# Performance work log

Measured on AMD Instinct MI355X. Metric: run time of the kernel, lower is better.

Reference implementation:

```python
import math
import jax, jax.numpy as jnp
import numpy as np

B, T, E, H = 4, 2048, 1024, 16
S = E // H
SCALE = 1.0 / math.sqrt(S)
LN_EPS = 1e-5


def setup_inputs() -> dict:
    key = jax.random.key(0)
    ks = jax.random.split(key, 5)
    w_std = 1.0 / math.sqrt(E)
    return {
        "x": jax.random.normal(ks[0], (B, T, E), jnp.float32),
        "Wq": jax.random.normal(ks[1], (E, E), jnp.float32) * w_std,
        "Wk": jax.random.normal(ks[2], (E, E), jnp.float32) * w_std,
        "Wv": jax.random.normal(ks[3], (E, E), jnp.float32) * w_std,
        "Wu": jax.random.normal(ks[4], (E, E), jnp.float32) * w_std,
        "bu": jnp.zeros((E,), jnp.float32),
        "q_gamma": jnp.ones((S,), jnp.float32),
        "q_beta": jnp.zeros((S,), jnp.float32),
        "k_gamma": jnp.ones((S,), jnp.float32),
        "k_beta": jnp.zeros((S,), jnp.float32),
    }


def _layernorm(x, gamma, beta):
    # normalize over last (head) dim, eps matches torch LayerNorm default
    mu = jnp.mean(x, axis=-1, keepdims=True)
    var = jnp.mean(jnp.square(x - mu), axis=-1, keepdims=True)
    return (x - mu) * jax.lax.rsqrt(var + LN_EPS) * gamma + beta


def reference(x, Wq, Wk, Wv, Wu, bu, q_gamma, q_beta, k_gamma, k_beta):
    b, t, e = x.shape
    h, s = H, S
    # torch Linear: y = x @ W^T ; split into heads [b, t, h, s]
    q = (x @ Wq.T).reshape(b, t, h, s)
    k = (x @ Wk.T).reshape(b, t, h, s)
    v = (x @ Wv.T).reshape(b, t, h, s)
    # kqnorm: LayerNorm over head dim s
    q = _layernorm(q, q_gamma, q_beta)
    k = _layernorm(k, k_gamma, k_beta)
    # scaled dot-product scores [b, h, t, t]
    dots = jnp.einsum("bthd,bThd->bhtT", q, k) * SCALE
    causal = jnp.tril(jnp.ones((t, t), dtype=bool))
    dots = jnp.where(causal, dots, jnp.finfo(dots.dtype).min)
    attn = jax.nn.softmax(dots, axis=-1)
    out = jnp.einsum("bhtT,bThd->bthd", attn, v).reshape(b, t, e)
    return out @ Wu.T + bu
```

## Files before the change

### kernel.cpp

```cpp
#include <hip/hip_runtime.h>
#include <hip/hip_bf16.h>
#include <stdint.h>
#include <stddef.h>


using bf16 = __hip_bfloat16;
typedef __attribute__((ext_vector_type(8))) short s16x8;
typedef __attribute__((ext_vector_type(4))) short s16x4;
typedef __attribute__((ext_vector_type(4))) float f32x4;

#define MFMA16(a, b, c) __builtin_amdgcn_mfma_f32_16x16x32_bf16((a), (b), (c), 0, 0, 0)

static __device__ __forceinline__ s16x8 ld8(const bf16* p) {
    return *reinterpret_cast<const s16x8*>(p);
}
static __device__ __forceinline__ s16x8 ld8s(const short* p) {
    return *reinterpret_cast<const s16x8*>(p);
}
static __device__ __forceinline__ s16x8 cvt8(const float* p) {
    f32x4 u = *reinterpret_cast<const f32x4*>(p);
    f32x4 v = *reinterpret_cast<const f32x4*>(p + 4);
    s16x8 r;
#pragma unroll
    for (int e = 0; e < 4; e++) {
        r[e]     = __builtin_bit_cast(short, __float2bfloat16(u[e]));
        r[e + 4] = __builtin_bit_cast(short, __float2bfloat16(v[e]));
    }
    return r;
}
static __device__ __forceinline__ unsigned int cvtpk(float lo, float hi) {
    unsigned int r;
    asm("v_cvt_pk_bf16_f32 %0, %1, %2" : "=v"(r) : "v"(lo), "v"(hi));
    return r;
}

static __device__ __forceinline__ void async16(short* lds, const bf16* g) {
    __builtin_amdgcn_global_load_lds(
        (const __attribute__((address_space(1))) unsigned int*)g,
        (__attribute__((address_space(3))) unsigned int*)lds, 16, 0, 0);
}

#define EE 1024

__global__ __launch_bounds__(256) void cvt_all(
    const float* __restrict__ w0, const float* __restrict__ w1,
    const float* __restrict__ w2, const float* __restrict__ w3,
    const float* __restrict__ x,
    bf16* __restrict__ o0, bf16* __restrict__ o1,
    bf16* __restrict__ o2, bf16* __restrict__ o3, bf16* __restrict__ xb)
{
    const int z = blockIdx.z;
    const float* s;
    bf16* d;
    if (z < 4) {
        s = (z == 0) ? w0 : (z == 1) ? w1 : (z == 2) ? w2 : w3;
        d = (z == 0) ? o0 : (z == 1) ? o1 : (z == 2) ? o2 : o3;
    } else {
        s = x  + (size_t)(z - 4) * 1048576;
        d = xb + (size_t)(z - 4) * 1048576;
    }
    size_t i = ((size_t)blockIdx.x * 256 + threadIdx.x) * 8;
    *reinterpret_cast<s16x8*>(d + i) = cvt8(s + i);
}

template <int AF32>
__global__ __launch_bounds__(256) void gemm_qkv_t(
    const float* __restrict__ xf, const bf16* __restrict__ xb,
    const bf16* __restrict__ Wq, const bf16* __restrict__ Wk, const bf16* __restrict__ Wv,
    bf16* __restrict__ Qb, bf16* __restrict__ Kb, bf16* __restrict__ Vb,
    const float* __restrict__ qg, const float* __restrict__ qbt,
    const float* __restrict__ kg, const float* __restrict__ kbt)
{
    const int z = blockIdx.z;
    const bf16* Bt = (z == 0) ? Wq : (z == 1) ? Wk : Wv;
    bf16* out      = (z == 0) ? Qb : (z == 1) ? Kb : Vb;
    const float* gamma = (z == 0) ? qg : kg;
    const float* beta  = (z == 0) ? qbt : kbt;
    const bool  ln     = (z < 2);
    const float oscale = (z == 0) ? 0.125f : 1.0f;

    constexpr int LASZ = AF32 ? 128 * 40 : 2 * 4096;
    __shared__ __align__(16) short lA[LASZ];
    __shared__ __align__(16) short lB[2 * 4096];

    const int tid  = threadIdx.x;
    const int lane = tid & 63;
    const int w    = tid >> 6;
    const int wr = w >> 1, wc = w & 1;
    const int lr = lane & 15, quad = lane >> 4;

    const int mi = blockIdx.x * 8 + (blockIdx.y & 7);
    const int ni = blockIdx.y >> 3;
    const int m0 = mi * 128;
    const int n0 = ni * 128;

    const int strow = w * 32 + (lane >> 2);
    const int stcol = (lane & 3) * 8;
    const bf16* bgl = Bt + (size_t)(n0 + strow) * EE + stcol;

    f32x4 acc[4][4];
#pragma unroll
    for (int i = 0; i < 4; i++)
#pragma unroll
        for (int j = 0; j < 4; j++) acc[i][j] = (f32x4){0.f, 0.f, 0.f, 0.f};

    if constexpr (AF32) {
        constexpr int SA = 40;
        const int sr  = tid >> 1;
        const int sc0 = (tid & 1) << 4;
        const float* ap = xf + (size_t)(m0 + sr) * EE + sc0;
        short* lap = lA + sr * SA + sc0;
        short* bl = lB + (w * 2) * 512;
        const short* lArd = lA + (wr * 64 + lr) * SA + quad * 8;
        const short* lBrd = lB + (wc * 64 + lr) * 32 + quad * 8;
        const bf16* bg = bgl;

        for (int kt = 0; kt < EE / 32; ++kt) {
            s16x8 a0 = cvt8(ap), a1 = cvt8(ap + 8);
            __syncthreads();
            *reinterpret_cast<s16x8*>(lap)     = a0;
            *reinterpret_cast<s16x8*>(lap + 8) = a1;
            async16(bl, bg);
            async16(bl + 512, bg + 16 * EE);
            ap += 32;
            bg += 32;
            __syncthreads();

            s16x8 af[4], bfr[4];
#pragma unroll
            for (int i = 0; i < 4; i++) af[i]  = ld8s(lArd + i * 16 * SA);
#pragma unroll
            for (int j = 0; j < 4; j++) bfr[j] = ld8s(lBrd + j * 16 * 32);
#pragma unroll
            for (int i = 0; i < 4; i++)
#pragma unroll
                for (int j = 0; j < 4; j++) acc[i][j] = MFMA16(af[i], bfr[j], acc[i][j]);
        }
    } else {
        const bf16* agl = xb + (size_t)(m0 + strow) * EE + stcol;
        short* const al0 = lA + w * 1024;
        short* const bl0 = lB + w * 1024;

#define QSTAGE(c, kt)                                                     \
    {                                                                     \
        short* al = al0 + (c) * 4096;                                     \
        short* bl = bl0 + (c) * 4096;                                     \
        const bf16* ag = agl + (kt) * 32;                                 \
        const bf16* bg = bgl + (kt) * 32;                                 \
        async16(al, ag); async16(al + 512, ag + 16 * EE);                 \
        async16(bl, bg); async16(bl + 512, bg + 16 * EE);                 \
    }

        QSTAGE(0, 0)
#pragma unroll 1
        for (int kt = 0; kt < EE / 32; ++kt) {
            const int c = kt & 1;
            if (kt < EE / 32 - 1) {
                QSTAGE(c ^ 1, kt + 1)
                asm volatile("s_waitcnt vmcnt(4)" ::: "memory");
            } else {
                asm volatile("s_waitcnt vmcnt(0)" ::: "memory");
            }
            __builtin_amdgcn_s_barrier();

            const short* lArd = lA + c * 4096 + (wr * 64 + lr) * 32 + quad * 8;
            const short* lBrd = lB + c * 4096 + (wc * 64 + lr) * 32 + quad * 8;
            s16x8 af[4], bfr[4];
#pragma unroll
            for (int i = 0; i < 4; i++) af[i]  = ld8s(lArd + i * 512);
#pragma unroll
            for (int j = 0; j < 4; j++) bfr[j] = ld8s(lBrd + j * 512);
            __builtin_amdgcn_sched_barrier(0);
            asm volatile("s_waitcnt lgkmcnt(0)" ::: "memory");
            __builtin_amdgcn_sched_barrier(0);
#pragma unroll
            for (int i = 0; i < 4; i++)
#pragma unroll
                for (int j = 0; j < 4; j++) acc[i][j] = MFMA16(af[i], bfr[j], acc[i][j]);
            __builtin_amdgcn_s_barrier();
        }
#undef QSTAGE
    }

    if (ln) {
        float g[4], bt[4];
#pragma unroll
        for (int j = 0; j < 4; j++) {
            g[j]  = gamma[j * 16 + lr];
            bt[j] = beta[j * 16 + lr];
        }
#pragma unroll
        for (int i = 0; i < 4; i++) {
#pragma unroll
            for (int r = 0; r < 4; r++) {
                float s1 = 0.f, s2 = 0.f;
#pragma unroll
                for (int j = 0; j < 4; j++) {
                    float v = acc[i][j][r];
                    s1 += v;
                    s2 += v * v;
                }
#pragma unroll
                for (int off = 1; off < 16; off <<= 1) {
                    s1 += __shfl_xor(s1, off);
                    s2 += __shfl_xor(s2, off);
                }
                float mu  = s1 * (1.f / 64.f);
                float var = s2 * (1.f / 64.f) - mu * mu;
                float rs  = rsqrtf(var + 1e-5f);
                int row = m0 + wr * 64 + i * 16 + quad * 4 + r;
#pragma unroll
                for (int j = 0; j < 4; j++) {
                    float v = ((acc[i][j][r] - mu) * rs * g[j] + bt[j]) * oscale;
                    out[(size_t)row * EE + n0 + wc * 64 + j * 16 + lr] = __float2bfloat16(v);
                }
            }
        }
    } else {
#pragma unroll
        for (int i = 0; i < 4; i++)
#pragma unroll
            for (int r = 0; r < 4; r++) {
                int row = m0 + wr * 64 + i * 16 + quad * 4 + r;
#pragma unroll
                for (int j = 0; j < 4; j++)
                    out[(size_t)row * EE + n0 + wc * 64 + j * 16 + lr] =
                        __float2bfloat16(acc[i][j][r]);
            }
    }
}

__global__ __launch_bounds__(512, 4) void flash(
    const bf16* __restrict__ Qb, const bf16* __restrict__ Kb,
    const bf16* __restrict__ Vb, bf16* __restrict__ Ob)
{
    const int flat = blockIdx.y * 8 + blockIdx.x;
    const int vid  = (flat & 7) * 64 + (flat >> 3);
    const int pr = vid & 7;
    const int bh = vid >> 3;
    const int b = bh >> 4, h = bh & 15;
    const int tid = threadIdx.x, lane = tid & 63, w = tid >> 6;
    const int lr = lane & 15, quad = lane >> 4;
    const size_t base = (size_t)b * 2048 * 1024 + h * 64;
    const float C  = 1.44269504088896340736f;
    const float M0 = 12.0f;

    __shared__ __align__(16) short VT[64 * 72];
    __shared__ __align__(16) short PT[128 * 72];
    __shared__ __align__(16) short KS[2][64 * 64];

    short* const prow = PT + (w * 16 + lr) * 72;
    const bf16* const kst = Kb + base + (size_t)(w * 8 + (lane >> 3)) * 1024 +
                            (((lane & 7) ^ (lane >> 3)) << 3);
    short* const kdst = &KS[0][0] + w * 512;
    const int kaddr0 = lr * 64 + ((quad ^ (lr & 7)) << 3);

#pragma unroll 1
    for (int ph = 0; ph < 2; ++ph) {
        const int qt = ph ? (15 - pr) : pr;
        const int tw = qt * 128 + w * 16;

        s16x8 qf[2];
#pragma unroll
        for (int ks = 0; ks < 2; ks++)
            qf[ks] = ld8(Qb + base + (size_t)(tw + lr) * 1024 + ks * 32 + quad * 8);

        f32x4 o[4];
#pragma unroll
        for (int j = 0; j < 4; j++) o[j] = (f32x4){0.f, 0.f, 0.f, 0.f};
        float lsum = 0.f;

        const int nkt = 2 * qt + 2;

        __syncthreads();
        s16x8 va0 = ld8(Vb + base + (size_t)lane * 1024 + w * 8);
        s16x8 vb0;
        async16(kdst, kst);

#define FTILE(KT, V0C, KCUR, V0N, KNXT)                                          \
    {                                                                            \
        const int kb = (KT) * 64;                                                \
        const bool active = (kb <= tw + 15);                                     \
        asm volatile("s_waitcnt vmcnt(0)" ::: "memory");      \
        __builtin_amdgcn_s_barrier();       \
        _Pragma("unroll")                                                        \
        for (int e = 0; e < 8; e++)                                              \
            VT[(w * 8 + e) * 72 + lane] = V0C[e];                                \
        const int kb2 = kb + 64;                                                 \
        if (kb2 < nkt * 64) {       \
            async16(kdst + (KNXT) * 4096, kst + (size_t)kb2 * 1024);             \
            V0N = ld8(Vb + base + (size_t)(kb2 + lane) * 1024 + w * 8);          \
        }                                                                        \
        if (active) {                                                            \
            const short* kc = &KS[KCUR][0];                                      \
            f32x4 sc[4];                                                         \
            _Pragma("unroll")                                                    \
            for (int jk = 0; jk < 4; jk++) sc[jk] = (f32x4){0.f, 0.f, 0.f, 0.f}; \
            __builtin_amdgcn_s_setprio(1);                                       \
            _Pragma("unroll")                                                    \
            for (int ks = 0; ks < 2; ks++)                                       \
                _Pragma("unroll")                                                \
                for (int jk = 0; jk < 4; jk++) {                                 \
                    s16x8 kf = ld8s(kc + jk * 1024 + (kaddr0 ^ (ks * 32)));      \
                    sc[jk] = MFMA16(kf, qf[ks], sc[jk]);                         \
                }                                                                \
            __builtin_amdgcn_s_setprio(0);                                       \
            if (kb + 63 > tw) {                  \
                const int qq = tw + lr;                                          \
                _Pragma("unroll")                                                \
                for (int jk = 0; jk < 4; jk++) {                                 \
                    const int k0 = kb + jk * 16 + quad * 4;                      \
                    float p0 = exp2f(fmaf(sc[jk][0], C, -M0));                   \
                    float p1 = exp2f(fmaf(sc[jk][1], C, -M0));                   \
                    float p2 = exp2f(fmaf(sc[jk][2], C, -M0));                   \
                    float p3 = exp2f(fmaf(sc[jk][3], C, -M0));                   \
                    if (k0 + 0 > qq) p0 = 0.f;                                   \
                    if (k0 + 1 > qq) p1 = 0.f;                                   \
                    if (k0 + 2 > qq) p2 = 0.f;                                   \
                    if (k0 + 3 > qq) p3 = 0.f;                                   \
                    lsum += (p0 + p1) + (p2 + p3);                               \
                    uint2 pk = {cvtpk(p0, p1), cvtpk(p2, p3)};                   \
                    *reinterpret_cast<uint2*>(prow + jk * 16 + quad * 4) = pk;   \
                }                                                                \
            } else {                                 \
                _Pragma("unroll")                                                \
                for (int jk = 0; jk < 4; jk++) {                                 \
                    float p0 = exp2f(fmaf(sc[jk][0], C, -M0));                   \
                    float p1 = exp2f(fmaf(sc[jk][1], C, -M0));                   \
                    float p2 = exp2f(fmaf(sc[jk][2], C, -M0));                   \
                    float p3 = exp2f(fmaf(sc[jk][3], C, -M0));                   \
                    lsum += (p0 + p1) + (p2 + p3);                               \
                    uint2 pk = {cvtpk(p0, p1), cvtpk(p2, p3)};                   \
                    *reinterpret_cast<uint2*>(prow + jk * 16 + quad * 4) = pk;   \
                }                                                                \
            }                                                                    \
        }                                                                        \
        asm volatile("s_waitcnt lgkmcnt(0)" ::: "memory");    \
        __builtin_amdgcn_s_barrier();                  \
        if (active) {                                                            \
            _Pragma("unroll")                                                    \
            for (int ks = 0; ks < 2; ks++) {                                     \
                s16x8 pf = ld8s(prow + ks * 32 + quad * 8);                      \
                s16x8 vf[4];                                                     \
                _Pragma("unroll")                                                \
                for (int j = 0; j < 4; j++)                                      \
                    vf[j] = ld8s(VT + (j * 16 + lr) * 72 + ks * 32 + quad * 8);  \
                __builtin_amdgcn_s_setprio(1);                                   \
                _Pragma("unroll")                                                \
                for (int j = 0; j < 4; j++)                                      \
                    o[j] = MFMA16(pf, vf[j], o[j]);                              \
                __builtin_amdgcn_s_setprio(0);                                   \
            }                                                                    \
        }                                                                        \
    }

#pragma unroll 1
        for (int kt = 0; kt < nkt; kt += 2) {
            FTILE(kt,     va0, 0, vb0, 1)
            FTILE(kt + 1, vb0, 1, va0, 0)
        }
#undef FTILE

        float l = lsum;
        l += __shfl_xor(l, 16);
        l += __shfl_xor(l, 32);
#pragma unroll
        for (int r = 0; r < 4; r++) {
            float inv = 1.f / __shfl(l, quad * 4 + r);
            int t = tw + quad * 4 + r;
#pragma unroll
            for (int j = 0; j < 4; j++)
                Ob[base + (size_t)t * 1024 + j * 16 + lr] =
                    __float2bfloat16(o[j][r] * inv);
        }
    }
}

__global__ __launch_bounds__(256) void gemm_bias(
    const bf16* __restrict__ A, const bf16* __restrict__ Bt,
    const float* __restrict__ bias, float* __restrict__ out)
{
    __shared__ __align__(16) short lA[2 * 4096];
    __shared__ __align__(16) short lB[2 * 4096];

    const int tid  = threadIdx.x;
    const int lane = tid & 63;
    const int w    = tid >> 6;
    const int wr = w >> 1, wc = w & 1;
    const int lr = lane & 15, quad = lane >> 4;

    const int mi = blockIdx.x * 8 + (blockIdx.y & 7);
    const int ni = blockIdx.y >> 3;
    const int m0 = mi * 128;
    const int n0 = ni * 128;

    const int strow = w * 32 + (lane >> 2);
    const int stcol = (lane & 3) * 8;
    const bf16* agl = A  + (size_t)(m0 + strow) * EE + stcol;
    const bf16* bgl = Bt + (size_t)(n0 + strow) * EE + stcol;
    short* const al0 = lA + w * 1024;
    short* const bl0 = lB + w * 1024;

    f32x4 acc[4][4];
#pragma unroll
    for (int i = 0; i < 4; i++)
#pragma unroll
        for (int j = 0; j < 4; j++) acc[i][j] = (f32x4){0.f, 0.f, 0.f, 0.f};

#define BSTAGE(c, kt)                                                     \
    {                                                                     \
        short* al = al0 + (c) * 4096;                                     \
        short* bl = bl0 + (c) * 4096;                                     \
        const bf16* ag = agl + (kt) * 32;                                 \
        const bf16* bg = bgl + (kt) * 32;                                 \
        async16(al, ag); async16(al + 512, ag + 16 * EE);                 \
        async16(bl, bg); async16(bl + 512, bg + 16 * EE);                 \
    }

    BSTAGE(0, 0)
#pragma unroll 1
    for (int kt = 0; kt < EE / 32; ++kt) {
        const int c = kt & 1;
        if (kt < EE / 32 - 1) {
            BSTAGE(c ^ 1, kt + 1)
            asm volatile("s_waitcnt vmcnt(4)" ::: "memory");
        } else {
            asm volatile("s_waitcnt vmcnt(0)" ::: "memory");
        }
        __builtin_amdgcn_s_barrier();

        const short* lArd = lA + c * 4096 + (wr * 64 + lr) * 32 + quad * 8;
        const short* lBrd = lB + c * 4096 + (wc * 64 + lr) * 32 + quad * 8;
        s16x8 af[4], bfr[4];
#pragma unroll
        for (int i = 0; i < 4; i++) af[i]  = ld8s(lArd + i * 512);
#pragma unroll
        for (int j = 0; j < 4; j++) bfr[j] = ld8s(lBrd + j * 512);
        __builtin_amdgcn_sched_barrier(0);
        asm volatile("s_waitcnt lgkmcnt(0)" ::: "memory");
        __builtin_amdgcn_sched_barrier(0);
#pragma unroll
        for (int i = 0; i < 4; i++)
#pragma unroll
            for (int j = 0; j < 4; j++) acc[i][j] = MFMA16(af[i], bfr[j], acc[i][j]);
        __builtin_amdgcn_s_barrier();
    }
#undef BSTAGE

    float bz[4];
#pragma unroll
    for (int j = 0; j < 4; j++)
        bz[j] = bias[n0 + wc * 64 + j * 16 + lr];
#pragma unroll
    for (int i = 0; i < 4; i++)
#pragma unroll
        for (int r = 0; r < 4; r++) {
            int row = m0 + wr * 64 + i * 16 + quad * 4 + r;
#pragma unroll
            for (int j = 0; j < 4; j++)
                out[(size_t)row * EE + n0 + wc * 64 + j * 16 + lr] =
                    acc[i][j][r] + bz[j];
        }
}

extern "C" void kernel_launch(void* const* d_in, const int* in_sizes, int n_in,
                              void* d_out, int out_size, void* d_ws, size_t ws_size,
                              hipStream_t stream)
{
    (void)in_sizes; (void)n_in; (void)out_size;
    const float* x   = (const float*)d_in[0];
    const float* Wq  = (const float*)d_in[1];
    const float* Wk  = (const float*)d_in[2];
    const float* Wv  = (const float*)d_in[3];
    const float* Wu  = (const float*)d_in[4];
    const float* bu  = (const float*)d_in[5];
    const float* qg  = (const float*)d_in[6];
    const float* qbt = (const float*)d_in[7];
    const float* kg  = (const float*)d_in[8];
    const float* kbt = (const float*)d_in[9];
    float* out = (float*)d_out;

    bf16* Qb  = (bf16*)d_ws;
    bf16* Kb  = Qb  + (size_t)8192 * 1024;
    bf16* Vb  = Kb  + (size_t)8192 * 1024;
    bf16* Wqb = Vb  + (size_t)8192 * 1024;
    bf16* Wkb = Wqb + (size_t)1024 * 1024;
    bf16* Wvb = Wkb + (size_t)1024 * 1024;
    bf16* Wub = Wvb + (size_t)1024 * 1024;
    bf16* xb  = Wub + (size_t)1024 * 1024;

    const size_t need = ((size_t)3 * 8192 * 1024 + 4 * 1024 * 1024 + 8192 * 1024) * 2;
    const bool fast = ws_size >= need;

    cvt_all<<<dim3(512, 1, fast ? 12 : 4), 256, 0, stream>>>(
        Wq, Wk, Wv, Wu, x, Wqb, Wkb, Wvb, Wub, xb);
    if (fast)
        gemm_qkv_t<0><<<dim3(8, 64, 3), 256, 0, stream>>>(
            x, xb, Wqb, Wkb, Wvb, Qb, Kb, Vb, qg, qbt, kg, kbt);
    else
        gemm_qkv_t<1><<<dim3(8, 64, 3), 256, 0, stream>>>(
            x, nullptr, Wqb, Wkb, Wvb, Qb, Kb, Vb, qg, qbt, kg, kbt);
    flash<<<dim3(8, 64), 512, 0, stream>>>(Qb, Kb, Vb, Qb);
    gemm_bias<<<dim3(8, 64), 256, 0, stream>>>(Qb, Wub, bu, out);
}
```

Baseline: 278.1 us.

## Split flash attention into 64-row query blocks with longest-first scheduling

The flash kernel moves from 512-thread blocks that each handle two paired 128-row query tiles to 256-thread blocks that each handle a single 64-row query tile. The grid grows from 512 to 2048 blocks, and query blocks are issued in descending order so the longest causal workloads start first. Each warp now loads twice as much K/V per tile, and the per-warp causal skip check is dropped. The aim is better load balance and occupancy from finer-grained work, at the cost of reloading K/V more often per query row, since each block has fewer query rows to reuse it.

```diff
diff --git a/kernel.cpp b/kernel.cpp
--- a/kernel.cpp
+++ b/kernel.cpp
@@ -230,14 +230,14 @@
     }
 }
 
-__global__ __launch_bounds__(512, 4) void flash(
+__global__ __launch_bounds__(256, 4) void flash(
     const bf16* __restrict__ Qb, const bf16* __restrict__ Kb,
     const bf16* __restrict__ Vb, bf16* __restrict__ Ob)
 {
-    const int flat = blockIdx.y * 8 + blockIdx.x;
-    const int vid  = (flat & 7) * 64 + (flat >> 3);
-    const int pr = vid & 7;
-    const int bh = vid >> 3;
+    const int flat = blockIdx.y * 32 + blockIdx.x;
+    const int vid  = (flat & 7) * 256 + (flat >> 3);
+    const int qb = 31 - (vid & 31);
+    const int bh = vid >> 5;
     const int b = bh >> 4, h = bh & 15;
     const int tid = threadIdx.x, lane = tid & 63, w = tid >> 6;
     const int lr = lane & 15, quad = lane >> 4;
@@ -246,52 +246,53 @@
     const float M0 = 12.0f;
 
     __shared__ __align__(16) short VT[64 * 72];
-    __shared__ __align__(16) short PT[128 * 72];
+    __shared__ __align__(16) short PT[64 * 72];
     __shared__ __align__(16) short KS[2][64 * 64];
 
     short* const prow = PT + (w * 16 + lr) * 72;
-    const bf16* const kst = Kb + base + (size_t)(w * 8 + (lane >> 3)) * 1024 +
+    const bf16* const kst = Kb + base + (size_t)(w * 16 + (lane >> 3)) * 1024 +
                             (((lane & 7) ^ (lane >> 3)) << 3);
-    short* const kdst = &KS[0][0] + w * 512;
+    short* const kdst = &KS[0][0] + w * 1024;
     const int kaddr0 = lr * 64 + ((quad ^ (lr & 7)) << 3);
 
-#pragma unroll 1
-    for (int ph = 0; ph < 2; ++ph) {
-        const int qt = ph ? (15 - pr) : pr;
-        const int tw = qt * 128 + w * 16;
-
-        s16x8 qf[2];
-#pragma unroll
-        for (int ks = 0; ks < 2; ks++)
-            qf[ks] = ld8(Qb + base + (size_t)(tw + lr) * 1024 + ks * 32 + quad * 8);
-
-        f32x4 o[4];
-#pragma unroll
-        for (int j = 0; j < 4; j++) o[j] = (f32x4){0.f, 0.f, 0.f, 0.f};
-        float lsum = 0.f;
-
-        const int nkt = 2 * qt + 2;
-
-        __syncthreads();
-        s16x8 va0 = ld8(Vb + base + (size_t)lane * 1024 + w * 8);
-        s16x8 vb0;
-        async16(kdst, kst);
-
-#define FTILE(KT, V0C, KCUR, V0N, KNXT)                                          \
+    const int tw = qb * 64 + w * 16;
+    const int nkt = qb + 1;
+
+    s16x8 qf[2];
+#pragma unroll
+    for (int ks = 0; ks < 2; ks++)
+        qf[ks] = ld8(Qb + base + (size_t)(tw + lr) * 1024 + ks * 32 + quad * 8);
+
+    f32x4 o[4];
+#pragma unroll
+    for (int j = 0; j < 4; j++) o[j] = (f32x4){0.f, 0.f, 0.f, 0.f};
+    float lsum = 0.f;
+
+    s16x8 va0 = ld8(Vb + base + (size_t)lane * 1024 + w * 8);
+    s16x8 va1 = ld8(Vb + base + (size_t)lane * 1024 + w * 8 + 32);
+    s16x8 vb0, vb1;
+    async16(kdst, kst);
+    async16(kdst + 512, kst + (size_t)8 * 1024);
+
+#define FTILE(KT, V0C, V1C, KCUR, V0N, V1N, KNXT)                                \
     {                                                                            \
         const int kb = (KT) * 64;                                                \
-        const bool active = (kb <= tw + 15);                                     \
         asm volatile("s_waitcnt vmcnt(0)" ::: "memory");      \
         __builtin_amdgcn_s_barrier();       \
         _Pragma("unroll")                                                        \
-        for (int e = 0; e < 8; e++)                                              \
-            VT[(w * 8 + e) * 72 + lane] = V0C[e];                                \
+        for (int e = 0; e < 8; e++) {                                            \
+            VT[(w * 8 + e) * 72 + lane]      = V0C[e];                           \
+            VT[(w * 8 + 32 + e) * 72 + lane] = V1C[e];                           \
+        }                                                                        \
         const int kb2 = kb + 64;                                                 \
         if (kb2 < nkt * 64) {       \
             async16(kdst + (KNXT) * 4096, kst + (size_t)kb2 * 1024);             \
+            async16(kdst + (KNXT) * 4096 + 512,                                  \
+                    kst + (size_t)(kb2 + 8) * 1024);                             \
             V0N = ld8(Vb + base + (size_t)(kb2 + lane) * 1024 + w * 8);          \
+            V1N = ld8(Vb + base + (size_t)(kb2 + lane) * 1024 + w * 8 + 32);     \
         }                                                                        \
-        if (active) {                                                            \
+        {                                                                        \
             const short* kc = &KS[KCUR][0];                                      \
             f32x4 sc[4];                                                         \
             _Pragma("unroll")                                                    \
@@ -337,7 +338,7 @@
         }                                                                        \
         asm volatile("s_waitcnt lgkmcnt(0)" ::: "memory");    \
         __builtin_amdgcn_s_barrier();                  \
-        if (active) {                                                            \
+        {                                                                        \
             _Pragma("unroll")                                                    \
             for (int ks = 0; ks < 2; ks++) {                                     \
                 s16x8 pf = ld8s(prow + ks * 32 + quad * 8);                      \
@@ -354,25 +355,28 @@
         }                                                                        \
     }
 
+    int kt = 0;
 #pragma unroll 1
-        for (int kt = 0; kt < nkt; kt += 2) {
-            FTILE(kt,     va0, 0, vb0, 1)
-            FTILE(kt + 1, vb0, 1, va0, 0)
-        }
+    for (; kt + 2 <= nkt; kt += 2) {
+        FTILE(kt,     va0, va1, 0, vb0, vb1, 1)
+        FTILE(kt + 1, vb0, vb1, 1, va0, va1, 0)
+    }
+    if (nkt & 1) {
+        FTILE(kt, va0, va1, 0, vb0, vb1, 1)
+    }
 #undef FTILE
 
-        float l = lsum;
-        l += __shfl_xor(l, 16);
-        l += __shfl_xor(l, 32);
-#pragma unroll
-        for (int r = 0; r < 4; r++) {
-            float inv = 1.f / __shfl(l, quad * 4 + r);
-            int t = tw + quad * 4 + r;
-#pragma unroll
-            for (int j = 0; j < 4; j++)
-                Ob[base + (size_t)t * 1024 + j * 16 + lr] =
-                    __float2bfloat16(o[j][r] * inv);
-        }
+    float l = lsum;
+    l += __shfl_xor(l, 16);
+    l += __shfl_xor(l, 32);
+#pragma unroll
+    for (int r = 0; r < 4; r++) {
+        float inv = 1.f / __shfl(l, quad * 4 + r);
+        int t = tw + quad * 4 + r;
+#pragma unroll
+        for (int j = 0; j < 4; j++)
+            Ob[base + (size_t)t * 1024 + j * 16 + lr] =
+                __float2bfloat16(o[j][r] * inv);
     }
 }
 
@@ -500,6 +504,6 @@
     else
         gemm_qkv_t<1><<<dim3(8, 64, 3), 256, 0, stream>>>(
             x, nullptr, Wqb, Wkb, Wvb, Qb, Kb, Vb, qg, qbt, kg, kbt);
-    flash<<<dim3(8, 64), 512, 0, stream>>>(Qb, Kb, Vb, Qb);
+    flash<<<dim3(32, 64), 256, 0, stream>>>(Qb, Kb, Vb, Qb);
     gemm_bias<<<dim3(8, 64), 256, 0, stream>>>(Qb, Wub, bu, out);
 }
```

After: 296.8 us. 1.07x slower.

## One query tile per flash block, double-buffer V in LDS, fold log2e into Q

Applied to the files above, without the earlier changes.

The flash kernel now launches one block per query tile, heaviest first, instead of pairing two tiles per block. This uses twice as many blocks and aims to improve load balance. V is double-buffered in LDS and prefetched two tiles ahead, which removes the mid-tile barrier between the softmax and PV stages. The log2(e) factor moves into the Q projection scale so the exp2 needs no FMA, and the fixed max offset M0 is dropped. Without that offset there is more risk of fp32 overflow on large scores, though LayerNorm bounds the scores here.

```diff
diff --git a/kernel.cpp b/kernel.cpp
--- a/kernel.cpp
+++ b/kernel.cpp
@@ -77,7 +77,7 @@
     const float* gamma = (z == 0) ? qg : kg;
     const float* beta  = (z == 0) ? qbt : kbt;
     const bool  ln     = (z < 2);
-    const float oscale = (z == 0) ? 0.125f : 1.0f;
+    const float oscale = (z == 0) ? 0.125f * 1.44269504088896340736f : 1.0f;
 
     constexpr int LASZ = AF32 ? 128 * 40 : 2 * 4096;
     __shared__ __align__(16) short lA[LASZ];
@@ -234,18 +234,16 @@
     const bf16* __restrict__ Qb, const bf16* __restrict__ Kb,
     const bf16* __restrict__ Vb, bf16* __restrict__ Ob)
 {
-    const int flat = blockIdx.y * 8 + blockIdx.x;
-    const int vid  = (flat & 7) * 64 + (flat >> 3);
-    const int pr = vid & 7;
-    const int bh = vid >> 3;
+    const int flat = blockIdx.y * 16 + blockIdx.x;
+    const int vid  = (flat & 7) * 128 + (flat >> 3);
+    const int bh = vid >> 4;
+    const int qt = 15 - (vid & 15);
     const int b = bh >> 4, h = bh & 15;
     const int tid = threadIdx.x, lane = tid & 63, w = tid >> 6;
     const int lr = lane & 15, quad = lane >> 4;
     const size_t base = (size_t)b * 2048 * 1024 + h * 64;
-    const float C  = 1.44269504088896340736f;
-    const float M0 = 12.0f;
-
-    __shared__ __align__(16) short VT[64 * 72];
+
+    __shared__ __align__(16) short VT[2][64 * 72];
     __shared__ __align__(16) short PT[128 * 72];
     __shared__ __align__(16) short KS[2][64 * 64];
 
@@ -255,42 +253,41 @@
     short* const kdst = &KS[0][0] + w * 512;
     const int kaddr0 = lr * 64 + ((quad ^ (lr & 7)) << 3);
 
-#pragma unroll 1
-    for (int ph = 0; ph < 2; ++ph) {
-        const int qt = ph ? (15 - pr) : pr;
-        const int tw = qt * 128 + w * 16;
-
-        s16x8 qf[2];
-#pragma unroll
-        for (int ks = 0; ks < 2; ks++)
-            qf[ks] = ld8(Qb + base + (size_t)(tw + lr) * 1024 + ks * 32 + quad * 8);
-
-        f32x4 o[4];
-#pragma unroll
-        for (int j = 0; j < 4; j++) o[j] = (f32x4){0.f, 0.f, 0.f, 0.f};
-        float lsum = 0.f;
-
-        const int nkt = 2 * qt + 2;
-
-        __syncthreads();
-        s16x8 va0 = ld8(Vb + base + (size_t)lane * 1024 + w * 8);
-        s16x8 vb0;
-        async16(kdst, kst);
-
-#define FTILE(KT, V0C, KCUR, V0N, KNXT)                                          \
+    const int tw = qt * 128 + w * 16;
+    const int nkt = 2 * qt + 2;
+
+    s16x8 qf[2];
+#pragma unroll
+    for (int ks = 0; ks < 2; ks++)
+        qf[ks] = ld8(Qb + base + (size_t)(tw + lr) * 1024 + ks * 32 + quad * 8);
+
+    f32x4 o[4];
+#pragma unroll
+    for (int j = 0; j < 4; j++) o[j] = (f32x4){0.f, 0.f, 0.f, 0.f};
+    float lsum = 0.f;
+
+    async16(kdst, kst);
+    s16x8 va = ld8(Vb + base + (size_t)lane * 1024 + w * 8);
+    s16x8 vb = ld8(Vb + base + (size_t)(64 + lane) * 1024 + w * 8);
+    asm volatile("s_waitcnt vmcnt(1)" ::: "memory");
+#pragma unroll
+    for (int e = 0; e < 8; e++)
+        VT[0][(w * 8 + e) * 72 + lane] = va[e];
+
+#define FTILE(KT, VWR, KCUR, VLD)                                                \
     {                                                                            \
         const int kb = (KT) * 64;                                                \
         const bool active = (kb <= tw + 15);                                     \
-        asm volatile("s_waitcnt vmcnt(0)" ::: "memory");      \
-        __builtin_amdgcn_s_barrier();       \
+        asm volatile("s_waitcnt vmcnt(0) lgkmcnt(0)" ::: "memory");              \
+        __builtin_amdgcn_s_barrier();    \
         _Pragma("unroll")                                                        \
-        for (int e = 0; e < 8; e++)                                              \
-            VT[(w * 8 + e) * 72 + lane] = V0C[e];                                \
-        const int kb2 = kb + 64;                                                 \
-        if (kb2 < nkt * 64) {       \
-            async16(kdst + (KNXT) * 4096, kst + (size_t)kb2 * 1024);             \
-            V0N = ld8(Vb + base + (size_t)(kb2 + lane) * 1024 + w * 8);          \
-        }                                                                        \
+        for (int e = 0; e < 8; e++)                     \
+            VT[(KCUR) ^ 1][(w * 8 + e) * 72 + lane] = VWR[e];                    \
+        const int kb2 = kb + 64, kb3 = kb + 128;                                 \
+        if (kb2 < nkt * 64)                \
+            async16(kdst + ((KCUR) ^ 1) * 4096, kst + (size_t)kb2 * 1024);       \
+        if (kb3 < nkt * 64)                                     \
+            VLD = ld8(Vb + base + (size_t)(kb3 + lane) * 1024 + w * 8);          \
         if (active) {                                                            \
             const short* kc = &KS[KCUR][0];                                      \
             f32x4 sc[4];                                                         \
@@ -310,10 +307,10 @@
                 _Pragma("unroll")                                                \
                 for (int jk = 0; jk < 4; jk++) {                                 \
                     const int k0 = kb + jk * 16 + quad * 4;                      \
-                    float p0 = exp2f(fmaf(sc[jk][0], C, -M0));                   \
-                    float p1 = exp2f(fmaf(sc[jk][1], C, -M0));                   \
-                    float p2 = exp2f(fmaf(sc[jk][2], C, -M0));                   \
-                    float p3 = exp2f(fmaf(sc[jk][3], C, -M0));                   \
+                    float p0 = exp2f(sc[jk][0]);                                 \
+                    float p1 = exp2f(sc[jk][1]);                                 \
+                    float p2 = exp2f(sc[jk][2]);                                 \
+                    float p3 = exp2f(sc[jk][3]);                                 \
                     if (k0 + 0 > qq) p0 = 0.f;                                   \
                     if (k0 + 1 > qq) p1 = 0.f;                                   \
                     if (k0 + 2 > qq) p2 = 0.f;                                   \
@@ -325,26 +322,25 @@
             } else {                                 \
                 _Pragma("unroll")                                                \
                 for (int jk = 0; jk < 4; jk++) {                                 \
-                    float p0 = exp2f(fmaf(sc[jk][0], C, -M0));                   \
-                    float p1 = exp2f(fmaf(sc[jk][1], C, -M0));                   \
-                    float p2 = exp2f(fmaf(sc[jk][2], C, -M0));                   \
-                    float p3 = exp2f(fmaf(sc[jk][3], C, -M0));                   \
+                    float p0 = exp2f(sc[jk][0]);                                 \
+                    float p1 = exp2f(sc[jk][1]);                                 \
+                    float p2 = exp2f(sc[jk][2]);                                 \
+                    float p3 = exp2f(sc[jk][3]);                                 \
                     lsum += (p0 + p1) + (p2 + p3);                               \
                     uint2 pk = {cvtpk(p0, p1), cvtpk(p2, p3)};                   \
                     *reinterpret_cast<uint2*>(prow + jk * 16 + quad * 4) = pk;   \
                 }                                                                \
             }                                                                    \
-        }                                                                        \
-        asm volatile("s_waitcnt lgkmcnt(0)" ::: "memory");    \
-        __builtin_amdgcn_s_barrier();                  \
-        if (active) {                                                            \
+            asm volatile("s_waitcnt lgkmcnt(0)" ::: "memory");  \
+            __builtin_amdgcn_sched_barrier(0);                                   \
             _Pragma("unroll")                                                    \
             for (int ks = 0; ks < 2; ks++) {                                     \
                 s16x8 pf = ld8s(prow + ks * 32 + quad * 8);                      \
                 s16x8 vf[4];                                                     \
                 _Pragma("unroll")                                                \
                 for (int j = 0; j < 4; j++)                                      \
-                    vf[j] = ld8s(VT + (j * 16 + lr) * 72 + ks * 32 + quad * 8);  \
+                    vf[j] = ld8s(&VT[KCUR][0] + (j * 16 + lr) * 72 +             \
+                                 ks * 32 + quad * 8);                            \
                 __builtin_amdgcn_s_setprio(1);                                   \
                 _Pragma("unroll")                                                \
                 for (int j = 0; j < 4; j++)                                      \
@@ -354,25 +350,25 @@
         }                                                                        \
     }
 
+    int kt = 0;
 #pragma unroll 1
-        for (int kt = 0; kt < nkt; kt += 2) {
-            FTILE(kt,     va0, 0, vb0, 1)
-            FTILE(kt + 1, vb0, 1, va0, 0)
-        }
+    for (; kt + 2 <= nkt; kt += 2) {
+        FTILE(kt,     vb, 0, va)
+        FTILE(kt + 1, va, 1, vb)
+    }
 #undef FTILE
 
-        float l = lsum;
-        l += __shfl_xor(l, 16);
-        l += __shfl_xor(l, 32);
-#pragma unroll
-        for (int r = 0; r < 4; r++) {
-            float inv = 1.f / __shfl(l, quad * 4 + r);
-            int t = tw + quad * 4 + r;
-#pragma unroll
-            for (int j = 0; j < 4; j++)
-                Ob[base + (size_t)t * 1024 + j * 16 + lr] =
-                    __float2bfloat16(o[j][r] * inv);
-        }
+    float l = lsum;
+    l += __shfl_xor(l, 16);
+    l += __shfl_xor(l, 32);
+#pragma unroll
+    for (int r = 0; r < 4; r++) {
+        float inv = 1.f / __shfl(l, quad * 4 + r);
+        int t = tw + quad * 4 + r;
+#pragma unroll
+        for (int j = 0; j < 4; j++)
+            Ob[base + (size_t)t * 1024 + j * 16 + lr] =
+                __float2bfloat16(o[j][r] * inv);
     }
 }
 
@@ -500,6 +496,6 @@
     else
         gemm_qkv_t<1><<<dim3(8, 64, 3), 256, 0, stream>>>(
             x, nullptr, Wqb, Wkb, Wvb, Qb, Kb, Vb, qg, qbt, kg, kbt);
-    flash<<<dim3(8, 64), 512, 0, stream>>>(Qb, Kb, Vb, Qb);
+    flash<<<dim3(16, 64), 512, 0, stream>>>(Qb, Kb, Vb, Qb);
     gemm_bias<<<dim3(8, 64), 256, 0, stream>>>(Qb, Wub, bu, out);
 }
```

After: 302.1 us. 8.6% more time.

## XOR-swizzle LDS tiles in GEMMs and flash, fold log2e into Q scale

Applied to the files above, without the earlier changes.

Switches the bf16 GEMM staging to an XOR-swizzled column layout, so that global-to-LDS async copies and fragment reads avoid LDS bank conflicts. The padded VT/PT buffers in flash attention become unpadded 64-wide rows with XOR swizzling, which shrinks LDS use and may allow higher occupancy. The log2(e) factor is folded into the Q output scale, so the softmax exp2 no longer needs a per-element fma. The fixed max offset M0 is dropped, which relies on the layernormed scores staying bounded so that exp2 cannot overflow.

```diff
diff --git a/kernel.cpp b/kernel.cpp
--- a/kernel.cpp
+++ b/kernel.cpp
@@ -77,7 +77,7 @@
     const float* gamma = (z == 0) ? qg : kg;
     const float* beta  = (z == 0) ? qbt : kbt;
     const bool  ln     = (z < 2);
-    const float oscale = (z == 0) ? 0.125f : 1.0f;
+    const float oscale = (z == 0) ? 0.125f * 1.44269504088896340736f : 1.0f;
 
     constexpr int LASZ = AF32 ? 128 * 40 : 2 * 4096;
     __shared__ __align__(16) short lA[LASZ];
@@ -95,7 +95,8 @@
     const int n0 = ni * 128;
 
     const int strow = w * 32 + (lane >> 2);
-    const int stcol = (lane & 3) * 8;
+    const int stcol = AF32 ? (lane & 3) * 8
+                           : (((lane & 3) ^ (strow & 3)) << 3);
     const bf16* bgl = Bt + (size_t)(n0 + strow) * EE + stcol;
 
     f32x4 acc[4][4];
@@ -152,6 +153,8 @@
     }
 
         QSTAGE(0, 0)
+        const int ard = (wr * 64 + lr) * 32 + ((quad ^ (lr & 3)) << 3);
+        const int brd = (wc * 64 + lr) * 32 + ((quad ^ (lr & 3)) << 3);
 #pragma unroll 1
         for (int kt = 0; kt < EE / 32; ++kt) {
             const int c = kt & 1;
@@ -163,8 +166,8 @@
             }
             __builtin_amdgcn_s_barrier();
 
-            const short* lArd = lA + c * 4096 + (wr * 64 + lr) * 32 + quad * 8;
-            const short* lBrd = lB + c * 4096 + (wc * 64 + lr) * 32 + quad * 8;
+            const short* lArd = lA + c * 4096 + ard;
+            const short* lBrd = lB + c * 4096 + brd;
             s16x8 af[4], bfr[4];
 #pragma unroll
             for (int i = 0; i < 4; i++) af[i]  = ld8s(lArd + i * 512);
@@ -242,18 +245,17 @@
     const int tid = threadIdx.x, lane = tid & 63, w = tid >> 6;
     const int lr = lane & 15, quad = lane >> 4;
     const size_t base = (size_t)b * 2048 * 1024 + h * 64;
-    const float C  = 1.44269504088896340736f;
-    const float M0 = 12.0f;
-
-    __shared__ __align__(16) short VT[64 * 72];
-    __shared__ __align__(16) short PT[128 * 72];
+
+    __shared__ __align__(16) short VT[64 * 64];
+    __shared__ __align__(16) short PT[128 * 64];
     __shared__ __align__(16) short KS[2][64 * 64];
 
-    short* const prow = PT + (w * 16 + lr) * 72;
+    short* const prow = PT + (w * 16 + lr) * 64;
+    const int lr7 = lr & 7;
     const bf16* const kst = Kb + base + (size_t)(w * 8 + (lane >> 3)) * 1024 +
                             (((lane & 7) ^ (lane >> 3)) << 3);
     short* const kdst = &KS[0][0] + w * 512;
-    const int kaddr0 = lr * 64 + ((quad ^ (lr & 7)) << 3);
+    const int kaddr0 = lr * 64 + ((quad ^ lr7) << 3);
 
 #pragma unroll 1
     for (int ph = 0; ph < 2; ++ph) {
@@ -284,8 +286,9 @@
         asm volatile("s_waitcnt vmcnt(0)" ::: "memory");      \
         __builtin_amdgcn_s_barrier();       \
         _Pragma("unroll")                                                        \
-        for (int e = 0; e < 8; e++)                                              \
-            VT[(w * 8 + e) * 72 + lane] = V0C[e];                                \
+        for (int e = 0; e < 8; e++)          \
+            VT[(w * 8 + e) * 64 + (((lane >> 3) ^ e) << 3) + (lane & 7)]         \
+                = V0C[e];                                                        \
         const int kb2 = kb + 64;                                                 \
         if (kb2 < nkt * 64) {       \
             async16(kdst + (KNXT) * 4096, kst + (size_t)kb2 * 1024);             \
@@ -310,28 +313,32 @@
                 _Pragma("unroll")                                                \
                 for (int jk = 0; jk < 4; jk++) {                                 \
                     const int k0 = kb + jk * 16 + quad * 4;                      \
-                    float p0 = exp2f(fmaf(sc[jk][0], C, -M0));                   \
-                    float p1 = exp2f(fmaf(sc[jk][1], C, -M0));                   \
-                    float p2 = exp2f(fmaf(sc[jk][2], C, -M0));                   \
-                    float p3 = exp2f(fmaf(sc[jk][3], C, -M0));                   \
+                    float p0 = exp2f(sc[jk][0]);                                 \
+                    float p1 = exp2f(sc[jk][1]);                                 \
+                    float p2 = exp2f(sc[jk][2]);                                 \
+                    float p3 = exp2f(sc[jk][3]);                                 \
                     if (k0 + 0 > qq) p0 = 0.f;                                   \
                     if (k0 + 1 > qq) p1 = 0.f;                                   \
                     if (k0 + 2 > qq) p2 = 0.f;                                   \
                     if (k0 + 3 > qq) p3 = 0.f;                                   \
                     lsum += (p0 + p1) + (p2 + p3);                               \
                     uint2 pk = {cvtpk(p0, p1), cvtpk(p2, p3)};                   \
-                    *reinterpret_cast<uint2*>(prow + jk * 16 + quad * 4) = pk;   \
+                    *reinterpret_cast<uint2*>(                                   \
+                        prow + (((jk * 2 + (quad >> 1)) ^ lr7) << 3) +           \
+                        ((quad & 1) << 2)) = pk;                                 \
                 }                                                                \
             } else {                                 \
                 _Pragma("unroll")                                                \
                 for (int jk = 0; jk < 4; jk++) {                                 \
-                    float p0 = exp2f(fmaf(sc[jk][0], C, -M0));                   \
-                    float p1 = exp2f(fmaf(sc[jk][1], C, -M0));                   \
-                    float p2 = exp2f(fmaf(sc[jk][2], C, -M0));                   \
-                    float p3 = exp2f(fmaf(sc[jk][3], C, -M0));                   \
+                    float p0 = exp2f(sc[jk][0]);                                 \
+                    float p1 = exp2f(sc[jk][1]);                                 \
+                    float p2 = exp2f(sc[jk][2]);                                 \
+                    float p3 = exp2f(sc[jk][3]);                                 \
                     lsum += (p0 + p1) + (p2 + p3);                               \
                     uint2 pk = {cvtpk(p0, p1), cvtpk(p2, p3)};                   \
-                    *reinterpret_cast<uint2*>(prow + jk * 16 + quad * 4) = pk;   \
+                    *reinterpret_cast<uint2*>(                                   \
+                        prow + (((jk * 2 + (quad >> 1)) ^ lr7) << 3) +           \
+                        ((quad & 1) << 2)) = pk;                                 \
                 }                                                                \
             }                                                                    \
         }                                                                        \
@@ -340,11 +347,12 @@
         if (active) {                                                            \
             _Pragma("unroll")                                                    \
             for (int ks = 0; ks < 2; ks++) {                                     \
-                s16x8 pf = ld8s(prow + ks * 32 + quad * 8);                      \
+                s16x8 pf = ld8s(prow + (((ks * 4 + quad) ^ lr7) << 3));          \
                 s16x8 vf[4];                                                     \
                 _Pragma("unroll")                                                \
                 for (int j = 0; j < 4; j++)                                      \
-                    vf[j] = ld8s(VT + (j * 16 + lr) * 72 + ks * 32 + quad * 8);  \
+                    vf[j] = ld8s(VT + (j * 16 + lr) * 64 +                       \
+                                 (((ks * 4 + quad) ^ lr7) << 3));                \
                 __builtin_amdgcn_s_setprio(1);                                   \
                 _Pragma("unroll")                                                \
                 for (int j = 0; j < 4; j++)                                      \
@@ -395,7 +403,7 @@
     const int n0 = ni * 128;
 
     const int strow = w * 32 + (lane >> 2);
-    const int stcol = (lane & 3) * 8;
+    const int stcol = (((lane & 3) ^ (strow & 3)) << 3);
     const bf16* agl = A  + (size_t)(m0 + strow) * EE + stcol;
     const bf16* bgl = Bt + (size_t)(n0 + strow) * EE + stcol;
     short* const al0 = lA + w * 1024;
@@ -418,6 +426,8 @@
     }
 
     BSTAGE(0, 0)
+    const int ard = (wr * 64 + lr) * 32 + ((quad ^ (lr & 3)) << 3);
+    const int brd = (wc * 64 + lr) * 32 + ((quad ^ (lr & 3)) << 3);
 #pragma unroll 1
     for (int kt = 0; kt < EE / 32; ++kt) {
         const int c = kt & 1;
@@ -429,8 +439,8 @@
         }
         __builtin_amdgcn_s_barrier();
 
-        const short* lArd = lA + c * 4096 + (wr * 64 + lr) * 32 + quad * 8;
-        const short* lBrd = lB + c * 4096 + (wc * 64 + lr) * 32 + quad * 8;
+        const short* lArd = lA + c * 4096 + ard;
+        const short* lBrd = lB + c * 4096 + brd;
         s16x8 af[4], bfr[4];
 #pragma unroll
         for (int i = 0; i < 4; i++) af[i]  = ld8s(lArd + i * 512);
```

After: 271.2 us. -2.5%, faster.
